# Performance work log

Hardware: AMD Instinct MI355X
Metric: run time of the kernel (lower is better)

The kernel has to match this reference:

```python
import jax, jax.numpy as jnp
import numpy as np

DEG = np.pi / 180.0
H_FOV = (-180.0 * DEG, 180.0 * DEG)   # azimuth fov (rad)
V_FOV = (-3.0 * DEG, 25.0 * DEG)      # elevation fov (rad), phi = -asin(z/r)
W = 2048  # int((h_fov[1]-h_fov[0]) / h_res), h_res = 360/2048 deg
H = 64    # int((v_fov[1]-v_fov[0]) / v_res), v_res = 28/64 deg
B = 8
N = 2_000_000


def setup_inputs() -> dict:
    key = jax.random.key(0)
    k1, k2, k3 = jax.random.split(key, 3)
    # realistic lidar-scale coordinates: wide xy spread, shallow z
    xyz = jax.random.normal(k1, (N, 3), jnp.float32) * jnp.array([30.0, 30.0, 3.0], jnp.float32)
    inten = jax.random.uniform(k2, (N, 1), dtype=jnp.float32)
    bs = jax.random.randint(k3, (N, 1), 0, B).astype(jnp.float32)  # batch idx stored as float col 0
    points = jnp.concatenate([bs, xyz, inten], axis=1)  # [N, 5]
    return {"points": points, "batch_size": B}


def reference(points, batch_size):
    # points: [N, 1+4] = (batch_idx, x, y, z, intensity)
    bs_idx = points[:, 0].astype(jnp.int32)
    xyz = points[:, 1:4]
    extra = points[:, 4:]

    # spherical projection: r, theta (azimuth, cw from +x), phi (elevation, cw from xy-plane)
    r = jnp.linalg.norm(xyz, axis=1, keepdims=True)                      # [N,1]
    theta = -jnp.arctan2(xyz[:, 1], xyz[:, 0])[:, None]                  # [N,1]
    phi = -jnp.arcsin(xyz[:, 2:3] / jnp.maximum(r, 1e-5))                # [N,1]

    u_n = (theta - H_FOV[0]) / (H_FOV[1] - H_FOV[0])                     # [N,1] normed col
    v_n = (phi - V_FOV[0]) / (V_FOV[1] - V_FOV[0])                       # [N,1] normed row

    mask = (u_n[:, 0] >= 0) & (u_n[:, 0] < 1) & (v_n[:, 0] >= 0) & (v_n[:, 0] < 1)

    u = (u_n[:, 0] * W).astype(jnp.int32)
    v = (v_n[:, 0] * H).astype(jnp.int32)
    # route masked-out points to an out-of-bounds index; scatter mode='drop' discards them
    u = jnp.where(mask, u, W)
    v = jnp.where(mask, v, H)

    # use_xyz=True: features = [xyz, rThetaPhi, raw_features] -> channels = 7
    features = jnp.concatenate([xyz, r, theta, phi, extra], axis=1)      # [N,7]

    rv = jnp.zeros((batch_size, H, W, features.shape[1]), points.dtype)
    rv = rv.at[bs_idx, v, u].set(features, mode='drop')
    return jnp.transpose(rv, (0, 3, 1, 2))  # [B, 7, H, W]
```

## Files before the change

kernel.cpp:

```cpp
#include <hip/hip_runtime.h>
#include <math.h>

#define W_IMG 2048
#define H_IMG 64
#define B_IMG 8
#define C_IMG 7
#define HW_IMG (H_IMG * W_IMG)
#define NPIX (B_IMG * HW_IMG)

typedef float v4f __attribute__((ext_vector_type(4)));

__device__ __forceinline__ float F(unsigned u) { return __uint_as_float(u); }
#define FMAF(a,b,c) __builtin_fmaf((a),(b),(c))

__device__ __forceinline__ float glibc_atanf(float x) {
    const float atanhi[4] = {F(0x3eed6338u), F(0x3f490fdau), F(0x3f7b985eu), F(0x3fc90fdau)};
    const float atanlo[4] = {F(0x31ac3769u), F(0x33222168u), F(0x33140fb4u), F(0x33a22168u)};
    const float aT0 = F(0x3eaaaaabu), aT1 = F(0xbe4ccccdu), aT2 = F(0x3e124925u),
                aT3 = F(0xbde38e38u), aT4 = F(0x3dba2e6eu), aT5 = F(0xbd9d8795u),
                aT6 = F(0x3d886b35u), aT7 = F(0xbd6ef16bu), aT8 = F(0x3d4bda59u),
                aT9 = F(0xbd15a221u), aT10 = F(0x3c8569d7u);

    unsigned hx = __float_as_uint(x);
    unsigned ix = hx & 0x7fffffffu;
    if (ix >= 0x4c800000u) {
        if (ix > 0x7f800000u) return x + x;
        float v = __fadd_rn(atanhi[3], atanlo[3]);
        return (hx >> 31) ? -v : v;
    }
    int id;
    float xr = x;
    if (ix < 0x3ee00000u) {
        if (ix < 0x31000000u) return x;
        id = -1;
    } else {
        xr = fabsf(x);
        if (ix < 0x3f980000u) {
            if (ix < 0x3f300000u) {
                id = 0;
                xr = __fdiv_rn(__fsub_rn(__fmul_rn(2.0f, xr), 1.0f),
                               __fadd_rn(2.0f, xr));
            } else {
                id = 1;
                xr = __fdiv_rn(__fsub_rn(xr, 1.0f), __fadd_rn(xr, 1.0f));
            }
        } else {
            if (ix < 0x401c0000u) {
                id = 2;
                xr = __fdiv_rn(__fsub_rn(xr, 1.5f),
                               __fadd_rn(1.0f, __fmul_rn(1.5f, xr)));
            } else {
                id = 3;
                xr = __fdiv_rn(-1.0f, xr);
            }
        }
    }
    float z = __fmul_rn(xr, xr);
    float w = __fmul_rn(z, z);
    float s1 = __fmul_rn(z, __fadd_rn(aT0, __fmul_rn(w, __fadd_rn(aT2,
               __fmul_rn(w, __fadd_rn(aT4, __fmul_rn(w, __fadd_rn(aT6,
               __fmul_rn(w, __fadd_rn(aT8, __fmul_rn(w, aT10)))))))))));
    float s2 = __fmul_rn(w, __fadd_rn(aT1, __fmul_rn(w, __fadd_rn(aT3,
               __fmul_rn(w, __fadd_rn(aT5, __fmul_rn(w, __fadd_rn(aT7,
               __fmul_rn(w, aT9)))))))));
    if (id < 0) return __fsub_rn(x, __fmul_rn(x, __fadd_rn(s1, s2)));
    float zz = __fsub_rn(atanhi[id],
               __fsub_rn(__fsub_rn(__fmul_rn(xr, __fadd_rn(s1, s2)), atanlo[id]), xr));
    return (hx >> 31) ? -zz : zz;
}

__device__ __forceinline__ float glibc_atan2f(float y, float x) {
    const float pi_o_2 = F(0x3fc90fdbu);
    const float pi     = F(0x40490fdbu);
    const float pi_lo  = F(0xb3bbbd2eu);
    unsigned hx = __float_as_uint(x), hy = __float_as_uint(y);
    unsigned ix = hx & 0x7fffffffu, iy = hy & 0x7fffffffu;
    if (ix > 0x7f800000u || iy > 0x7f800000u) return x + y;
    if (hx == 0x3f800000u) return glibc_atanf(y);
    unsigned m = ((hy >> 31) & 1u) | ((hx >> 30) & 2u);
    if (iy == 0) {
        switch (m) {
            case 0: case 1: return y;
            case 2: return pi;
            default: return -pi;
        }
    }
    if (ix == 0) return (m & 1u) ? -pi_o_2 : pi_o_2;
    if (ix == 0x7f800000u) {
        if (iy == 0x7f800000u) {
            switch (m) {
                case 0: return F(0x3f490fdbu);
                case 1: return -F(0x3f490fdbu);
                case 2: return __fmul_rn(3.0f, F(0x3f490fdbu));
                default: return -__fmul_rn(3.0f, F(0x3f490fdbu));
            }
        } else {
            switch (m) {
                case 0: return 0.0f;
                case 1: return -0.0f;
                case 2: return pi;
                default: return -pi;
            }
        }
    }
    if (iy == 0x7f800000u) return (m & 1u) ? -pi_o_2 : pi_o_2;

    int k = ((int)iy - (int)ix) >> 23;
    float z;
    if (k > 26) {
        z = __fadd_rn(pi_o_2, __fmul_rn(0.5f, pi_lo));
        m &= 1u;
    } else if (k < -26 && (hx >> 31)) {
        z = 0.0f;
    } else {
        z = glibc_atanf(fabsf(__fdiv_rn(y, x)));
    }
    switch (m) {
        case 0: return z;
        case 1: return __uint_as_float(__float_as_uint(z) ^ 0x80000000u);
        case 2: return __fsub_rn(pi, __fsub_rn(z, pi_lo));
        default: return __fsub_rn(__fsub_rn(z, pi_lo), pi);
    }
}

struct Proj {
    float theta, phi;
    int   pix;
    bool  in_image;
};

#define H0F   ((float)(-3.14159265358979323846))
#define SPANH ((float)( 6.28318530717958647692))
#define V0F   ((float)(-3.0 * 3.14159265358979323846 / 180.0))
#define SPANV ((float)((25.0 * 3.14159265358979323846 / 180.0) - \
                       (-3.0 * 3.14159265358979323846 / 180.0)))
#define RHc   (1.0f / SPANH)
#define RVc   (1.0f / SPANV)

__device__ __forceinline__ Proj project_exact(float x, float y, float zr, float bsf) {
    Proj p;
    p.theta = -glibc_atan2f(y, x);
    float s  = __fsqrt_rn(FMAF(-zr, zr, 1.0f));
    float d  = __fadd_rn(1.0f, s);
    p.phi = -__fmul_rn(2.0f, glibc_atan2f(zr, d));

    float u_n = __fmul_rn(__fsub_rn(p.theta, H0F), RHc);
    float v_n = __fmul_rn(__fsub_rn(p.phi,   V0F), RVc);
    p.in_image = (u_n >= 0.0f) && (u_n < 1.0f) && (v_n >= 0.0f) && (v_n < 1.0f);
    p.pix = -1;
    if (p.in_image) {
        int u = (int)__fmul_rn(u_n, (float)W_IMG);
        int v = (int)__fmul_rn(v_n, (float)H_IMG);
        int b = (int)bsf;
        if (u < W_IMG && v < H_IMG) {
            p.pix = (b * H_IMG + v) * W_IMG + u;
        } else {
            p.in_image = false;
        }
    }
    return p;
}

__device__ __forceinline__ float norm_r(float x, float y, float z) {
    return __fsqrt_rn(FMAF(z, z, FMAF(y, y, __fmul_rn(x, x))));
}

__device__ __forceinline__ float atan01(float t) {
    float q = t * t;
    float p =          -0.0117212f;
    p = FMAF(q, p,      0.05265332f);
    p = FMAF(q, p,     -0.11643287f);
    p = FMAF(q, p,      0.19354346f);
    p = FMAF(q, p,     -0.33262347f);
    p = FMAF(q, p,      0.99997726f);
    return t * p;
}

__device__ __forceinline__ void fast_angles(float x, float y, float zr,
                                            float* theta, float* phi) {
    float ax = fabsf(x), ay = fabsf(y);
    float mx = fmaxf(ax, ay), mn = fminf(ax, ay);
    float t = (mx > 0.0f) ? (mn / mx) : 0.0f;
    float a = atan01(t);
    if (ay > ax) a = 1.57079632679f - a;
    if (x < 0.0f) a = 3.14159265359f - a;
    *theta = (y < 0.0f) ? a : -a;

    float az  = fabsf(zr);
    float arg = az / __fsqrt_rn(FMAF(-zr, zr, 1.0f));
    float pa  = atan01(arg);
    *phi = (zr >= 0.0f) ? -pa : pa;
}

#define MU 0.06f
#define MV 0.025f

__global__ void __launch_bounds__(256)
scatter_winner(const float* __restrict__ pts, int* __restrict__ winner, int n) {
    int t = blockIdx.x * blockDim.x + threadIdx.x;
    if (t >= n) return;
    int i = n - 1 - t;
    const float* q = pts + (size_t)i * 5;
    float bsf = q[0], x = q[1], y = q[2], z = q[3];

    float r  = norm_r(x, y, z);
    float zr = __fdiv_rn(z, fmaxf(r, 1e-5f));
    if (zr > 0.05240f || zr < -0.42270f) return;

    float th_a, ph_a;
    fast_angles(x, y, zr, &th_a, &ph_a);
    float uf = (th_a - H0F) * (RHc * (float)W_IMG);
    float vf = (ph_a - V0F) * (RVc * (float)H_IMG);
    float ulo = floorf(uf - MU), uhi = floorf(uf + MU);
    float vlo = floorf(vf - MV), vhi = floorf(vf + MV);

    int pix;
    if (ulo == uhi && vlo == vhi) {
        int u = (int)ulo, v = (int)vlo;
        if (u < 0 || u >= W_IMG || v < 0 || v >= H_IMG) return;
        pix = ((int)bsf * H_IMG + v) * W_IMG + u;
    } else {
        Proj p = project_exact(x, y, zr, bsf);
        if (!p.in_image) return;
        pix = p.pix;
    }

    if (winner[pix] >= i) return;
    atomicMax(&winner[pix], i);
}

__global__ void __launch_bounds__(256, 4)
write_output(const float* __restrict__ pts, const int* __restrict__ winner,
             float* __restrict__ out) {
    int t  = blockIdx.x * blockDim.x + threadIdx.x;
    int p0 = t * 4;
    if (p0 >= NPIX) return;

    int4 w4 = *(const int4*)(winner + p0);
    int wis[4] = {w4.x, w4.y, w4.z, w4.w};

    float qx[4], qy[4], qz[4], qi[4];
#pragma unroll
    for (int k = 0; k < 4; ++k) {
        if (wis[k] >= 0) {
            const float* q = pts + (size_t)wis[k] * 5;
            qx[k] = q[1]; qy[k] = q[2]; qz[k] = q[3]; qi[k] = q[4];
        }
    }

    float fc[C_IMG][4];
#pragma unroll
    for (int c = 0; c < C_IMG; ++c)
#pragma unroll
        for (int k = 0; k < 4; ++k) fc[c][k] = 0.f;

#pragma unroll
    for (int k = 0; k < 4; ++k) {
        if (wis[k] >= 0) {
            float x = qx[k], y = qy[k], z = qz[k];
            float r  = norm_r(x, y, z);
            float zr = __fdiv_rn(z, fmaxf(r, 1e-5f));
            float th, ph;
            fast_angles(x, y, zr, &th, &ph);
            fc[0][k] = x; fc[1][k] = y; fc[2][k] = z;
            fc[3][k] = r; fc[4][k] = th; fc[5][k] = ph;
            fc[6][k] = qi[k];
        }
    }

    int b  = p0 >> 17;
    int hw = p0 & (HW_IMG - 1);
    size_t base = (size_t)b * C_IMG * HW_IMG + hw;
#pragma unroll
    for (int c = 0; c < C_IMG; ++c) {
        v4f v = {fc[c][0], fc[c][1], fc[c][2], fc[c][3]};
        __builtin_nontemporal_store(v, (v4f*)(out + base + (size_t)c * HW_IMG));
    }
}

extern "C" void kernel_launch(void* const* d_in, const int* in_sizes, int n_in,
                              void* d_out, int out_size, void* d_ws, size_t ws_size,
                              hipStream_t stream) {
    const float* pts = (const float*)d_in[0];
    int n = in_sizes[0] / 5;
    int* winner = (int*)d_ws;
    float* out = (float*)d_out;

    scatter_winner<<<(n + 255) / 256, 256, 0, stream>>>(pts, winner, n);

    int pthreads = NPIX / 4;
    write_output<<<(pthreads + 255) / 256, 256, 0, stream>>>(pts, winner, out);
}
```

Before: 144.8 us.

## Use accurate atan2 projection with tight ambiguity margins and 8 pixels per thread

The polynomial atan approximation is replaced with library atan2f for theta and a half-angle atan2 form for phi. This lets the ambiguity margins shrink, so fewer points fall through to the exact glibc-matching projection. The winner lookup for unambiguous points is issued before the branch. The output kernel now handles 8 pixels per thread instead of 4, which raises register pressure and doubles the library trig work per thread.

```diff
diff --git a/kernel.cpp b/kernel.cpp
--- a/kernel.cpp
+++ b/kernel.cpp
@@ -9,6 +9,7 @@
 #define NPIX (B_IMG * HW_IMG)
 
 typedef float v4f __attribute__((ext_vector_type(4)));
+typedef int   v4i __attribute__((ext_vector_type(4)));
 
 __device__ __forceinline__ float F(unsigned u) { return __uint_as_float(u); }
 #define FMAF(a,b,c) __builtin_fmaf((a),(b),(c))
@@ -165,35 +166,8 @@
     return __fsqrt_rn(FMAF(z, z, FMAF(y, y, __fmul_rn(x, x))));
 }
 
-__device__ __forceinline__ float atan01(float t) {
-    float q = t * t;
-    float p =          -0.0117212f;
-    p = FMAF(q, p,      0.05265332f);
-    p = FMAF(q, p,     -0.11643287f);
-    p = FMAF(q, p,      0.19354346f);
-    p = FMAF(q, p,     -0.33262347f);
-    p = FMAF(q, p,      0.99997726f);
-    return t * p;
-}
-
-__device__ __forceinline__ void fast_angles(float x, float y, float zr,
-                                            float* theta, float* phi) {
-    float ax = fabsf(x), ay = fabsf(y);
-    float mx = fmaxf(ax, ay), mn = fminf(ax, ay);
-    float t = (mx > 0.0f) ? (mn / mx) : 0.0f;
-    float a = atan01(t);
-    if (ay > ax) a = 1.57079632679f - a;
-    if (x < 0.0f) a = 3.14159265359f - a;
-    *theta = (y < 0.0f) ? a : -a;
-
-    float az  = fabsf(zr);
-    float arg = az / __fsqrt_rn(FMAF(-zr, zr, 1.0f));
-    float pa  = atan01(arg);
-    *phi = (zr >= 0.0f) ? -pa : pa;
-}
-
-#define MU 0.06f
-#define MV 0.025f
+#define MU 0.002f
+#define MV 0.0004f
 
 __global__ void __launch_bounds__(256)
 scatter_winner(const float* __restrict__ pts, int* __restrict__ winner, int n) {
@@ -207,25 +181,37 @@
     float zr = __fdiv_rn(z, fmaxf(r, 1e-5f));
     if (zr > 0.05240f || zr < -0.42270f) return;
 
-    float th_a, ph_a;
-    fast_angles(x, y, zr, &th_a, &ph_a);
-    float uf = (th_a - H0F) * (RHc * (float)W_IMG);
-    float vf = (ph_a - V0F) * (RVc * (float)H_IMG);
-    float ulo = floorf(uf - MU), uhi = floorf(uf + MU);
-    float vlo = floorf(vf - MV), vhi = floorf(vf + MV);
+    float th = -atan2f(y, x);
+    float s  = __fsqrt_rn(FMAF(-zr, zr, 1.0f));
+    float d  = __fadd_rn(1.0f, s);
+    float ph = -__fmul_rn(2.0f, atan2f(zr, d));
+
+    float u_n = __fmul_rn(__fsub_rn(th, H0F), RHc);
+    float v_n = __fmul_rn(__fsub_rn(ph, V0F), RVc);
+    float uf  = __fmul_rn(u_n, (float)W_IMG);
+    float vf  = __fmul_rn(v_n, (float)H_IMG);
+
+    float fu = uf - floorf(uf);
+    float fv = vf - floorf(vf);
+    bool amb = (fu < MU) | (fu > 1.0f - MU) | (fv < MV) | (fv > 1.0f - MV);
+
+    bool in_img = (u_n >= 0.0f) & (u_n < 1.0f) & (v_n >= 0.0f) & (v_n < 1.0f);
+    int u = (int)uf, v = (int)vf;
+    int pix_fast = ((int)bsf * H_IMG + v) * W_IMG + u;
+    int w_pre = (in_img & !amb) ? winner[pix_fast] : -1;
 
     int pix;
-    if (ulo == uhi && vlo == vhi) {
-        int u = (int)ulo, v = (int)vlo;
-        if (u < 0 || u >= W_IMG || v < 0 || v >= H_IMG) return;
-        pix = ((int)bsf * H_IMG + v) * W_IMG + u;
+    if (!amb) {
+        if (!in_img) return;
+        if (u >= W_IMG || v >= H_IMG) return;
+        pix = pix_fast;
+        if (w_pre >= i) return;
     } else {
         Proj p = project_exact(x, y, zr, bsf);
         if (!p.in_image) return;
         pix = p.pix;
-    }
-
-    if (winner[pix] >= i) return;
+        if (winner[pix] >= i) return;
+    }
     atomicMax(&winner[pix], i);
 }
 
@@ -233,35 +219,38 @@
 write_output(const float* __restrict__ pts, const int* __restrict__ winner,
              float* __restrict__ out) {
     int t  = blockIdx.x * blockDim.x + threadIdx.x;
-    int p0 = t * 4;
+    int p0 = t * 8;
     if (p0 >= NPIX) return;
 
-    int4 w4 = *(const int4*)(winner + p0);
-    int wis[4] = {w4.x, w4.y, w4.z, w4.w};
-
-    float qx[4], qy[4], qz[4], qi[4];
-#pragma unroll
-    for (int k = 0; k < 4; ++k) {
+    v4i wa = *(const v4i*)(winner + p0);
+    v4i wb = *(const v4i*)(winner + p0 + 4);
+    int wis[8] = {wa.x, wa.y, wa.z, wa.w, wb.x, wb.y, wb.z, wb.w};
+
+    float qx[8], qy[8], qz[8], qi[8];
+#pragma unroll
+    for (int k = 0; k < 8; ++k) {
         if (wis[k] >= 0) {
             const float* q = pts + (size_t)wis[k] * 5;
             qx[k] = q[1]; qy[k] = q[2]; qz[k] = q[3]; qi[k] = q[4];
         }
     }
 
-    float fc[C_IMG][4];
+    float fc[C_IMG][8];
 #pragma unroll
     for (int c = 0; c < C_IMG; ++c)
 #pragma unroll
-        for (int k = 0; k < 4; ++k) fc[c][k] = 0.f;
-
-#pragma unroll
-    for (int k = 0; k < 4; ++k) {
+        for (int k = 0; k < 8; ++k) fc[c][k] = 0.f;
+
+#pragma unroll
+    for (int k = 0; k < 8; ++k) {
         if (wis[k] >= 0) {
             float x = qx[k], y = qy[k], z = qz[k];
             float r  = norm_r(x, y, z);
             float zr = __fdiv_rn(z, fmaxf(r, 1e-5f));
-            float th, ph;
-            fast_angles(x, y, zr, &th, &ph);
+            float th = -atan2f(y, x);
+            float s  = __fsqrt_rn(FMAF(-zr, zr, 1.0f));
+            float dd = __fadd_rn(1.0f, s);
+            float ph = -__fmul_rn(2.0f, atan2f(zr, dd));
             fc[0][k] = x; fc[1][k] = y; fc[2][k] = z;
             fc[3][k] = r; fc[4][k] = th; fc[5][k] = ph;
             fc[6][k] = qi[k];
@@ -273,8 +262,10 @@
     size_t base = (size_t)b * C_IMG * HW_IMG + hw;
 #pragma unroll
     for (int c = 0; c < C_IMG; ++c) {
-        v4f v = {fc[c][0], fc[c][1], fc[c][2], fc[c][3]};
-        __builtin_nontemporal_store(v, (v4f*)(out + base + (size_t)c * HW_IMG));
+        v4f va = {fc[c][0], fc[c][1], fc[c][2], fc[c][3]};
+        v4f vb = {fc[c][4], fc[c][5], fc[c][6], fc[c][7]};
+        __builtin_nontemporal_store(va, (v4f*)(out + base + (size_t)c * HW_IMG));
+        __builtin_nontemporal_store(vb, (v4f*)(out + base + (size_t)c * HW_IMG + 4));
     }
 }
 
@@ -288,6 +279,6 @@
 
     scatter_winner<<<(n + 255) / 256, 256, 0, stream>>>(pts, winner, n);
 
-    int pthreads = NPIX / 4;
+    int pthreads = NPIX / 8;
     write_output<<<(pthreads + 255) / 256, 256, 0, stream>>>(pts, winner, out);
 }
```

After: 147.9 us. 2.1% more time.
